# Performance work log

Hardware: AMD Instinct MI355X
Metric: run time of the kernel (lower is better)

## Reference

```python
import jax, jax.numpy as jnp
import numpy as np
from jax import lax

C = 64          # grid_channels
RGB = 3         # rgb_channels
D = 128         # conditioning_dim
NUM_CLASSES = 1000
HIDDEN = 256    # hypernet hidden
NUM_STEPS = 32
TOT1 = C * C * 9


def setup_inputs() -> dict:
    key = jax.random.key(0)
    ks = jax.random.split(key, 20)
    s = 0.02
    B, H, W = 32, 64, 64
    return {
        "class_labels": jax.random.randint(ks[0], (B,), 0, NUM_CLASSES),
        "initial_grid": jax.random.normal(ks[1], (B, C, H, W), jnp.float32) * 0.1,
        "emb": jax.random.normal(ks[2], (NUM_CLASSES, D), jnp.float32) * s,
        "hw1": jax.random.normal(ks[3], (D, HIDDEN), jnp.float32) * s,
        "hb1": jnp.zeros((HIDDEN,), jnp.float32),
        "hw2": jax.random.normal(ks[4], (HIDDEN, HIDDEN), jnp.float32) * s,
        "hb2": jnp.zeros((HIDDEN,), jnp.float32),
        "hw3": jax.random.normal(ks[5], (HIDDEN, 2 * TOT1), jnp.float32) * s,
        "hb3": jnp.zeros((2 * TOT1,), jnp.float32),
        "f1w1": jax.random.normal(ks[6], (D, D), jnp.float32) * s,
        "f1b1": jnp.zeros((D,), jnp.float32),
        "f1w2": jax.random.normal(ks[7], (D, 2 * C), jnp.float32) * s,
        "f1b2": jnp.concatenate([jnp.ones((C,), jnp.float32), jnp.zeros((C,), jnp.float32)]),
        "f2w1": jax.random.normal(ks[8], (D, D), jnp.float32) * s,
        "f2b1": jnp.zeros((D,), jnp.float32),
        "f2w2": jax.random.normal(ks[9], (D, 2 * C), jnp.float32) * s,
        "f2b2": jnp.concatenate([jnp.ones((C,), jnp.float32), jnp.zeros((C,), jnp.float32)]),
        "blend": jnp.float32(0.5),
    }


def _conv_circ_one(x, w):
    # x: [C,H,W], w: [Cout,Cin,3,3]; circular pad then VALID conv == padding=1 circular
    xp = jnp.pad(x, ((0, 0), (1, 1), (1, 1)), mode='wrap')
    return lax.conv_general_dilated(xp[None], w, (1, 1), 'VALID')[0]

_bconv = jax.vmap(_conv_circ_one)  # per-sample dynamic weights over batch


def _film_params(cond, w1, b1, w2, b2):
    p = jax.nn.relu(cond @ w1 + b1) @ w2 + b2  # [B, 2C]
    return p[:, :C, None, None], p[:, C:, None, None]


def reference(class_labels, initial_grid, emb, hw1, hb1, hw2, hb2, hw3, hb3,
              f1w1, f1b1, f1w2, f1b2, f2w1, f2b1, f2w2, f2b2, blend):
    cond = emb[class_labels]                       # [B, D]
    h = jax.nn.relu(cond @ hw1 + hb1)
    h = jax.nn.relu(h @ hw2 + hb2)
    weights = h @ hw3 + hb3                        # [B, 2*C*C*9]
    B = cond.shape[0]
    w1 = weights[:, :TOT1].reshape(B, C, C, 3, 3)
    w2 = weights[:, TOT1:].reshape(B, C, C, 3, 3)
    g1, be1 = _film_params(cond, f1w1, f1b1, f1w2, f1b2)
    g2, be2 = _film_params(cond, f2w1, f2b1, f2w2, f2b2)
    blend_s = jax.nn.sigmoid(blend)

    def step(grid, _):
        u = jax.nn.relu(g1 * _bconv(grid, w1) + be1)
        u = jax.nn.relu(g2 * _bconv(u, w2) + be2)
        grid = (1 - blend_s) * grid + blend_s * u
        rgb = jax.nn.sigmoid(grid[:, :RGB])
        return grid, rgb

    _, traj = lax.scan(step, initial_grid, None, length=NUM_STEPS)  # [T,B,3,H,W]
    return traj[-1], traj
```

## Files before the change

kernel.cpp:

```cpp
#include <hip/hip_runtime.h>


typedef __attribute__((ext_vector_type(8))) short short8;
typedef __attribute__((ext_vector_type(4))) float f32x4;
typedef __attribute__((ext_vector_type(8))) unsigned short us8;

__device__ __forceinline__ unsigned short f2bf(float f) {
  unsigned int u = __builtin_bit_cast(unsigned int, f);
  u = (u + 0x7FFFu + ((u >> 16) & 1u)) >> 16;
  return (unsigned short)u;
}
__device__ __forceinline__ float bf2f(unsigned short h) {
  unsigned int u = ((unsigned int)h) << 16;
  return __builtin_bit_cast(float, u);
}

__device__ __forceinline__ void gl_lds16(const void* g, void* l) {
  __builtin_amdgcn_global_load_lds((const __attribute__((address_space(1))) void*)g,
                                   (__attribute__((address_space(3))) void*)l, 16, 0, 0);
}

__global__ void hyper_kernel(const int* __restrict__ labels, const float* __restrict__ emb,
                             const float* __restrict__ hw1, const float* __restrict__ hb1,
                             const float* __restrict__ hw2, const float* __restrict__ hb2,
                             float* __restrict__ h2T) {
  __shared__ float cond[128];
  __shared__ float h1[256];
  const int s = blockIdx.x, j = threadIdx.x;
  if (j < 128) cond[j] = emb[(size_t)labels[s] * 128 + j];
  __syncthreads();
  float a = hb1[j];
  for (int k = 0; k < 128; ++k) a += cond[k] * hw1[k * 256 + j];
  h1[j] = fmaxf(a, 0.f);
  __syncthreads();
  float a2 = hb2[j];
  for (int k = 0; k < 256; ++k) a2 += h1[k] * hw2[k * 256 + j];
  h2T[j * 32 + s] = fmaxf(a2, 0.f);
}

__global__ void film_kernel(const int* __restrict__ labels, const float* __restrict__ emb,
                            const float* __restrict__ f1w1, const float* __restrict__ f1b1,
                            const float* __restrict__ f1w2, const float* __restrict__ f1b2,
                            const float* __restrict__ f2w1, const float* __restrict__ f2b1,
                            const float* __restrict__ f2w2, const float* __restrict__ f2b2,
                            float* __restrict__ film) {
  __shared__ float cond[128];
  __shared__ float hid[128];
  const int s = blockIdx.x, which = blockIdx.y, j = threadIdx.x;
  const float* W1 = which ? f2w1 : f1w1;
  const float* B1 = which ? f2b1 : f1b1;
  const float* W2 = which ? f2w2 : f1w2;
  const float* B2 = which ? f2b2 : f1b2;
  cond[j] = emb[(size_t)labels[s] * 128 + j];
  __syncthreads();
  float a = B1[j];
  for (int k = 0; k < 128; ++k) a += cond[k] * W1[k * 128 + j];
  hid[j] = fmaxf(a, 0.f);
  __syncthreads();
  float p = B2[j];
  for (int k = 0; k < 128; ++k) p += hid[k] * W2[k * 128 + j];
  film[(size_t)((which * 2 + (j >> 6)) * 32 + s) * 64 + (j & 63)] = p;
}

__launch_bounds__(256)
__global__ void wgen_kernel(const float* __restrict__ h2T, const float* __restrict__ hw3,
                            const float* __restrict__ hb3, unsigned short* __restrict__ W) {
  __shared__ float h2l[8192];
  const int t = threadIdx.x;
  for (int i = t; i < 8192; i += 256) h2l[i] = h2T[i];
  __syncthreads();
  const int j  = blockIdx.x * 64 + (t & 63);
  const int sg = t >> 6;
  float acc[8];
  #pragma unroll
  for (int i = 0; i < 8; ++i) acc[i] = 0.f;
  const float* hp = &h2l[sg * 8];
  #pragma unroll 4
  for (int k = 0; k < 256; ++k) {
    const float w = hw3[(size_t)k * 73728 + j];
    const float4 hA = *(const float4*)(hp + k * 32);
    const float4 hB = *(const float4*)(hp + k * 32 + 4);
    acc[0] += hA.x * w; acc[1] += hA.y * w; acc[2] += hA.z * w; acc[3] += hA.w * w;
    acc[4] += hB.x * w; acc[5] += hB.y * w; acc[6] += hB.z * w; acc[7] += hB.w * w;
  }
  const float bias = hb3[j];
  const int cv = j / 36864;
  const int r  = j - cv * 36864;
  const int co = r / 576;
  const int r2 = r - co * 576;
  const int ci = r2 / 9;
  const int tap = r2 - ci * 9;
  const int sw = (co * 64 + ci) ^ ((co & 7) << 3);
  #pragma unroll
  for (int i = 0; i < 8; ++i) {
    const int s2 = sg * 8 + i;
    W[(size_t)((s2 * 2 + cv) * 9 + tap) * 4096 + sw] = f2bf(acc[i] + bias);
  }
}

__global__ void init_kernel(const float* __restrict__ gin, unsigned short* __restrict__ g0) {
  __shared__ float lds[64][65];
  const int b = blockIdx.x >> 6, y = blockIdx.x & 63;
  const int t = threadIdx.x;
  {
    const int ci = t >> 2, xq = t & 3;
    const float* base = gin + (size_t)((b * 64 + ci) * 64 + y) * 64;
    #pragma unroll
    for (int q = 0; q < 4; ++q) {
      const int x0 = (xq + q * 4) * 4;
      const float4 v = *(const float4*)(base + x0);
      lds[ci][x0+0] = v.x; lds[ci][x0+1] = v.y; lds[ci][x0+2] = v.z; lds[ci][x0+3] = v.w;
    }
  }
  __syncthreads();
  const int x = t >> 2, cq = t & 3, ci0 = cq * 16;
  us8 lo, hi;
  #pragma unroll
  for (int i = 0; i < 8; ++i) lo[i] = f2bf(lds[ci0 + i][x]);
  #pragma unroll
  for (int i = 0; i < 8; ++i) hi[i] = f2bf(lds[ci0 + 8 + i][x]);
  char* dbase = (char*)(g0 + (size_t)(b * 64 + y) * 4096);
  const int o = x * 128 + ci0 * 2, sw = (x & 7) << 4;
  *(us8*)(dbase + (o ^ sw)) = lo;
  *(us8*)(dbase + ((o + 16) ^ sw)) = hi;
}

template<int WHICH>
__launch_bounds__(512, 2)
__global__ void conv_kernel(const unsigned short* __restrict__ Wall,
                            const unsigned short* __restrict__ src,
                            unsigned short* __restrict__ dst,
                            const unsigned short* __restrict__ gold,
                            const float* __restrict__ film,
                            const float* __restrict__ blendp,
                            float* __restrict__ out, int t) {
  __shared__ unsigned short in_lds[10 * 4096];
  __shared__ unsigned short w_lds[9 * 4096];
  const int tid  = threadIdx.x;
  const int wid  = tid >> 6;
  const int lane = tid & 63;
  const int l15  = lane & 15;
  const int lhi  = lane >> 4;
  const int s    = blockIdx.x >> 3;
  const int y0   = (blockIdx.x & 7) * 8;

  const unsigned short* srcs = src + (size_t)s * 262144;
  const unsigned short* Wb   = Wall + (size_t)((s * 2 + WHICH) * 9) * 4096;

  #pragma unroll
  for (int q = 0; q < 10; ++q) {
    const int c   = q * 8 + wid;
    const int row = c >> 3, part = c & 7;
    const int gy  = (y0 + row + 63) & 63;
    gl_lds16(srcs + gy * 4096 + part * 512 + lane * 8, &in_lds[row * 4096 + part * 512]);
  }
  #pragma unroll
  for (int q = 0; q < 9; ++q) {
    const int c = q * 8 + wid;
    gl_lds16(Wb + c * 512 + lane * 8, &w_lds[c * 512]);
  }
  asm volatile("s_waitcnt vmcnt(0)" ::: "memory");
  __syncthreads();

  f32x4 acc[4][4];
  #pragma unroll
  for (int m = 0; m < 4; ++m)
    #pragma unroll
    for (int n = 0; n < 4; ++n)
      #pragma unroll
      for (int j = 0; j < 4; ++j) acc[m][n][j] = 0.f;

  #pragma unroll
  for (int tap = 0; tap < 9; ++tap) {
    const int ky = tap / 3, kx = tap % 3;
    short8 af[4][2], bfr[4][2];
    #pragma unroll
    for (int m = 0; m < 4; ++m) {
      const int co = m * 16 + l15;
      #pragma unroll
      for (int kk = 0; kk < 2; ++kk) {
        const int off = tap * 8192 + ((co * 128 + kk * 64 + lhi * 16) ^ ((co & 7) << 4));
        af[m][kk] = *(const short8*)((const char*)w_lds + off);
      }
    }
    const int r = wid + ky;
    #pragma unroll
    for (int n = 0; n < 4; ++n) {
      const int xs = (n * 16 + l15 + kx + 63) & 63;
      #pragma unroll
      for (int kk = 0; kk < 2; ++kk) {
        const int off = r * 8192 + ((xs * 128 + kk * 64 + lhi * 16) ^ ((xs & 7) << 4));
        bfr[n][kk] = *(const short8*)((const char*)in_lds + off);
      }
    }
    #pragma unroll
    for (int kk = 0; kk < 2; ++kk)
      #pragma unroll
      for (int m = 0; m < 4; ++m)
        #pragma unroll
        for (int n = 0; n < 4; ++n)
          acc[m][n] = __builtin_amdgcn_mfma_f32_16x16x32_bf16(af[m][kk], bfr[n][kk], acc[m][n], 0, 0, 0);
  }

  const int y = y0 + wid;
  const float* fg = film + WHICH * 2 * 2048;
  const float* fb = fg + 2048;
  float bs = 0.f, obs = 0.f;
  if (WHICH == 1) { bs = 1.f / (1.f + expf(-blendp[0])); obs = 1.f - bs; }
  unsigned short* drow = dst + (size_t)s * 262144 + y * 4096;
  const unsigned short* grow = (WHICH == 1) ? (gold + (size_t)s * 262144 + y * 4096) : (const unsigned short*)nullptr;

  #pragma unroll
  for (int m = 0; m < 4; ++m) {
    const int co0 = m * 16 + lhi * 4;
    const float4 g  = *(const float4*)&fg[s * 64 + co0];
    const float4 be = *(const float4*)&fb[s * 64 + co0];
    #pragma unroll
    for (int n = 0; n < 4; ++n) {
      const int x = n * 16 + l15;
      const int off = (x * 128 + co0 * 2) ^ ((x & 7) << 4);
      const f32x4 v = acc[m][n];
      const float u0 = fmaxf(g.x * v[0] + be.x, 0.f);
      const float u1 = fmaxf(g.y * v[1] + be.y, 0.f);
      const float u2 = fmaxf(g.z * v[2] + be.z, 0.f);
      const float u3 = fmaxf(g.w * v[3] + be.w, 0.f);
      if (WHICH == 0) {
        ushort4 pk; pk.x = f2bf(u0); pk.y = f2bf(u1); pk.z = f2bf(u2); pk.w = f2bf(u3);
        *(ushort4*)((char*)drow + off) = pk;
      } else {
        const ushort4 od = *(const ushort4*)((const char*)grow + off);
        const float g0 = obs * bf2f(od.x) + bs * u0;
        const float g1 = obs * bf2f(od.y) + bs * u1;
        const float g2 = obs * bf2f(od.z) + bs * u2;
        const float g3 = obs * bf2f(od.w) + bs * u3;
        ushort4 pk; pk.x = f2bf(g0); pk.y = f2bf(g1); pk.z = f2bf(g2); pk.w = f2bf(g3);
        *(ushort4*)((char*)drow + off) = pk;
        if (co0 == 0) {
          const float r0 = 1.f / (1.f + expf(-g0));
          const float r1 = 1.f / (1.f + expf(-g1));
          const float r2 = 1.f / (1.f + expf(-g2));
          float* ob = out + 393216 + (size_t)((t * 32 + s) * 3) * 4096 + y * 64 + x;
          ob[0] = r0; ob[4096] = r1; ob[8192] = r2;
          if (t == 31) {
            float* o2 = out + (size_t)(s * 3) * 4096 + y * 64 + x;
            o2[0] = r0; o2[4096] = r1; o2[8192] = r2;
          }
        }
      }
    }
  }
}

extern "C" void kernel_launch(void* const* d_in, const int* in_sizes, int n_in,
                              void* d_out, int out_size, void* d_ws, size_t ws_size,
                              hipStream_t stream) {
  (void)in_sizes; (void)n_in; (void)out_size; (void)ws_size;
  const int*   labels = (const int*)d_in[0];
  const float* gin    = (const float*)d_in[1];
  const float* emb    = (const float*)d_in[2];
  const float* hw1    = (const float*)d_in[3];
  const float* hb1    = (const float*)d_in[4];
  const float* hw2    = (const float*)d_in[5];
  const float* hb2    = (const float*)d_in[6];
  const float* hw3    = (const float*)d_in[7];
  const float* hb3    = (const float*)d_in[8];
  const float* f1w1   = (const float*)d_in[9];
  const float* f1b1   = (const float*)d_in[10];
  const float* f1w2   = (const float*)d_in[11];
  const float* f1b2   = (const float*)d_in[12];
  const float* f2w1   = (const float*)d_in[13];
  const float* f2b1   = (const float*)d_in[14];
  const float* f2w2   = (const float*)d_in[15];
  const float* f2b2   = (const float*)d_in[16];
  const float* blend  = (const float*)d_in[17];
  float* out = (float*)d_out;

  char* ws = (char*)d_ws;
  unsigned short* grid0 = (unsigned short*)(ws + (size_t)0);
  unsigned short* grid1 = (unsigned short*)(ws + (size_t)16777216);
  unsigned short* ubuf  = (unsigned short*)(ws + (size_t)33554432);
  unsigned short* Wbuf  = (unsigned short*)(ws + (size_t)50331648);
  float* h2T  = (float*)(ws + (size_t)55050240);
  float* film = (float*)(ws + (size_t)55083008);

  hyper_kernel<<<32, 256, 0, stream>>>(labels, emb, hw1, hb1, hw2, hb2, h2T);
  film_kernel<<<dim3(32, 2), 128, 0, stream>>>(labels, emb, f1w1, f1b1, f1w2, f1b2,
                                               f2w1, f2b1, f2w2, f2b2, film);
  wgen_kernel<<<1152, 256, 0, stream>>>(h2T, hw3, hb3, Wbuf);
  init_kernel<<<2048, 256, 0, stream>>>(gin, grid0);

  for (int t = 0; t < 32; ++t) {
    unsigned short* gi = (t & 1) ? grid1 : grid0;
    unsigned short* go = (t & 1) ? grid0 : grid1;
    conv_kernel<0><<<256, 512, 0, stream>>>(Wbuf, gi, ubuf, nullptr, film, nullptr, nullptr, t);
    conv_kernel<1><<<256, 512, 0, stream>>>(Wbuf, ubuf, go, gi, film, blend, out, t);
  }
}
```

Measured before the change: 1.430 ms.

## Double-buffer wgen loads with two columns per thread; remap conv block order

The weight-generation kernel now computes two output columns per thread with float2 loads of hw3. It prefetches them through a software double buffer of 8 rows, so each LDS read of h2 feeds twice as many FMAs and global latency is hidden, and it launches half as many blocks. The conv kernels remap blockIdx so consecutive blocks cover different samples at the same row band rather than eight row bands of one sample. That spreads per-sample weight and input traffic across CUs and L2 channels. The cost is more registers in wgen and fewer blocks there.

```diff
diff --git a/kernel.cpp b/kernel.cpp
--- a/kernel.cpp
+++ b/kernel.cpp
@@ -69,32 +69,73 @@
   const int t = threadIdx.x;
   for (int i = t; i < 8192; i += 256) h2l[i] = h2T[i];
   __syncthreads();
-  const int j  = blockIdx.x * 64 + (t & 63);
-  const int sg = t >> 6;
-  float acc[8];
-  #pragma unroll
-  for (int i = 0; i < 8; ++i) acc[i] = 0.f;
-  const float* hp = &h2l[sg * 8];
-  #pragma unroll 4
-  for (int k = 0; k < 256; ++k) {
-    const float w = hw3[(size_t)k * 73728 + j];
-    const float4 hA = *(const float4*)(hp + k * 32);
-    const float4 hB = *(const float4*)(hp + k * 32 + 4);
-    acc[0] += hA.x * w; acc[1] += hA.y * w; acc[2] += hA.z * w; acc[3] += hA.w * w;
-    acc[4] += hB.x * w; acc[5] += hB.y * w; acc[6] += hB.z * w; acc[7] += hB.w * w;
-  }
-  const float bias = hb3[j];
-  const int cv = j / 36864;
-  const int r  = j - cv * 36864;
-  const int co = r / 576;
-  const int r2 = r - co * 576;
-  const int ci = r2 / 9;
-  const int tap = r2 - ci * 9;
-  const int sw = (co * 64 + ci) ^ ((co & 7) << 3);
-  #pragma unroll
-  for (int i = 0; i < 8; ++i) {
-    const int s2 = sg * 8 + i;
-    W[(size_t)((s2 * 2 + cv) * 9 + tap) * 4096 + sw] = f2bf(acc[i] + bias);
+  const int lane = t & 63, sg = t >> 6;
+  const int j0 = blockIdx.x * 128 + lane * 2;
+  const float* __restrict__ gp = hw3 + j0;
+  const float* __restrict__ hp = h2l + sg * 8;
+
+  float acc[16];
+  #pragma unroll
+  for (int i = 0; i < 16; ++i) acc[i] = 0.f;
+
+  float2 bufA[8], bufB[8];
+  #pragma unroll
+  for (int u = 0; u < 8; ++u) bufA[u] = *(const float2*)(gp + (size_t)u * 73728);
+
+  #pragma unroll 1
+  for (int kc = 0; kc < 256; kc += 16) {
+    #pragma unroll
+    for (int u = 0; u < 8; ++u) bufB[u] = *(const float2*)(gp + (size_t)(kc + 8 + u) * 73728);
+    #pragma unroll
+    for (int u = 0; u < 8; ++u) {
+      const float4 hA = *(const float4*)(hp + (kc + u) * 32);
+      const float4 hB = *(const float4*)(hp + (kc + u) * 32 + 4);
+      const float2 wv = bufA[u];
+      acc[0]  += hA.x * wv.x; acc[1]  += hA.x * wv.y;
+      acc[2]  += hA.y * wv.x; acc[3]  += hA.y * wv.y;
+      acc[4]  += hA.z * wv.x; acc[5]  += hA.z * wv.y;
+      acc[6]  += hA.w * wv.x; acc[7]  += hA.w * wv.y;
+      acc[8]  += hB.x * wv.x; acc[9]  += hB.x * wv.y;
+      acc[10] += hB.y * wv.x; acc[11] += hB.y * wv.y;
+      acc[12] += hB.z * wv.x; acc[13] += hB.z * wv.y;
+      acc[14] += hB.w * wv.x; acc[15] += hB.w * wv.y;
+    }
+    if (kc + 16 < 256) {
+      #pragma unroll
+      for (int u = 0; u < 8; ++u) bufA[u] = *(const float2*)(gp + (size_t)(kc + 16 + u) * 73728);
+    }
+    #pragma unroll
+    for (int u = 0; u < 8; ++u) {
+      const float4 hA = *(const float4*)(hp + (kc + 8 + u) * 32);
+      const float4 hB = *(const float4*)(hp + (kc + 8 + u) * 32 + 4);
+      const float2 wv = bufB[u];
+      acc[0]  += hA.x * wv.x; acc[1]  += hA.x * wv.y;
+      acc[2]  += hA.y * wv.x; acc[3]  += hA.y * wv.y;
+      acc[4]  += hA.z * wv.x; acc[5]  += hA.z * wv.y;
+      acc[6]  += hA.w * wv.x; acc[7]  += hA.w * wv.y;
+      acc[8]  += hB.x * wv.x; acc[9]  += hB.x * wv.y;
+      acc[10] += hB.y * wv.x; acc[11] += hB.y * wv.y;
+      acc[12] += hB.z * wv.x; acc[13] += hB.z * wv.y;
+      acc[14] += hB.w * wv.x; acc[15] += hB.w * wv.y;
+    }
+  }
+
+  #pragma unroll
+  for (int c = 0; c < 2; ++c) {
+    const int j  = j0 + c;
+    const float bias = hb3[j];
+    const int cv = j / 36864;
+    const int r  = j - cv * 36864;
+    const int co = r / 576;
+    const int r2 = r - co * 576;
+    const int ci = r2 / 9;
+    const int tap = r2 - ci * 9;
+    const int sw = (co * 64 + ci) ^ ((co & 7) << 3);
+    #pragma unroll
+    for (int i = 0; i < 8; ++i) {
+      const int s2 = sg * 8 + i;
+      W[(size_t)((s2 * 2 + cv) * 9 + tap) * 4096 + sw] = f2bf(acc[i * 2 + c] + bias);
+    }
   }
 }
 
@@ -141,8 +182,9 @@
   const int lane = tid & 63;
   const int l15  = lane & 15;
   const int lhi  = lane >> 4;
-  const int s    = blockIdx.x >> 3;
-  const int y0   = (blockIdx.x & 7) * 8;
+  const int b    = blockIdx.x;
+  const int s    = (b & 7) + 8 * ((b >> 3) & 3);
+  const int y0   = (b >> 5) * 8;
 
   const unsigned short* srcs = src + (size_t)s * 262144;
   const unsigned short* Wb   = Wall + (size_t)((s * 2 + WHICH) * 9) * 4096;
@@ -286,7 +328,7 @@
   hyper_kernel<<<32, 256, 0, stream>>>(labels, emb, hw1, hb1, hw2, hb2, h2T);
   film_kernel<<<dim3(32, 2), 128, 0, stream>>>(labels, emb, f1w1, f1b1, f1w2, f1b2,
                                                f2w1, f2b1, f2w2, f2b2, film);
-  wgen_kernel<<<1152, 256, 0, stream>>>(h2T, hw3, hb3, Wbuf);
+  wgen_kernel<<<576, 256, 0, stream>>>(h2T, hw3, hb3, Wbuf);
   init_kernel<<<2048, 256, 0, stream>>>(gin, grid0);
 
   for (int t = 0; t < 32; ++t) {
```

After: 1.224 ms. 1.17x faster.
